# Kernel tuning notes

Measured on AMD Instinct MI355X. Metric: run time of the kernel, lower is better.

Reference implementation:

```python
import jax, jax.numpy as jnp
import numpy as np

DIM = 4096
HIDDEN = 11008
B, S = 4, 2048


def setup_inputs() -> dict:
    key = jax.random.key(0)
    k_x, k_g, k_u, k_d = jax.random.split(key, 4)
    x = jax.random.normal(k_x, (B, S, DIM), dtype=jnp.float32)
    # int8-range quantized weights, stored as int32 per spec (values in [-127, 127])
    w_gate = jax.random.randint(k_g, (HIDDEN, DIM), -127, 128, dtype=jnp.int32)
    w_up = jax.random.randint(k_u, (HIDDEN, DIM), -127, 128, dtype=jnp.int32)
    w_down = jax.random.randint(k_d, (DIM, HIDDEN), -127, 128, dtype=jnp.int32)
    # per-tensor scales (realistic small magnitudes)
    scale_gate = jnp.float32(0.01)
    scale_up = jnp.float32(0.01)
    scale_down = jnp.float32(0.01)
    return {
        "x": x,
        "w_gate": w_gate,
        "w_up": w_up,
        "w_down": w_down,
        "scale_gate": scale_gate,
        "scale_up": scale_up,
        "scale_down": scale_down,
    }


def _qlinear(x, w_int, scale):
    # faithful to QuantizedLinear.forward: dequantize then F.linear (x @ w.T)
    w = w_int.astype(x.dtype) * scale
    return jnp.einsum("bsd,hd->bsh", x, w)


def reference(x, w_gate, w_up, w_down, scale_gate, scale_up, scale_down):
    x_gate = _qlinear(x, w_gate, scale_gate)      # [B,S,HIDDEN]
    x_up = _qlinear(x, w_up, scale_up)            # [B,S,HIDDEN]
    x_mid = jax.nn.silu(x_gate) * x_up            # SwiGLU
    x_out = _qlinear(x_mid, w_down, scale_down)   # [B,S,DIM]
    return x_out
```

## Files before the change

### kernel.cpp

```cpp
#include <hip/hip_runtime.h>
#include <hip/hip_bf16.h>
#include <cstdint>
#include <cstddef>

#define DIM 4096
#define HIDDEN 11008
#define MTOK 8192

typedef __bf16 bf16x8 __attribute__((ext_vector_type(8)));
typedef float floatx4 __attribute__((ext_vector_type(4)));

__device__ __forceinline__ unsigned short f2bf(float f) {
    union { float f; unsigned int u; } v; v.f = f;
    unsigned int r = v.u + 0x7FFFu + ((v.u >> 16) & 1u);
    return (unsigned short)(r >> 16);
}

__device__ __forceinline__ void gload16(const void* g, void* l) {
    __builtin_amdgcn_global_load_lds(
        (const __attribute__((address_space(1))) unsigned int*)g,
        (__attribute__((address_space(3))) unsigned int*)l,
        16, 0, 0);
}

__device__ __forceinline__ floatx4 mfma16(bf16x8 a, bf16x8 b, floatx4 c) {
    return __builtin_amdgcn_mfma_f32_16x16x32_bf16(a, b, c, 0, 0, 0);
}


__global__ void cvt_f32_bf16(const float4* __restrict__ in, ushort4* __restrict__ out, int n4) {
    int i = blockIdx.x * 256 + threadIdx.x;
    if (i < n4) {
        float4 v = in[i];
        ushort4 o;
        o.x = f2bf(v.x); o.y = f2bf(v.y); o.z = f2bf(v.z); o.w = f2bf(v.w);
        out[i] = o;
    }
}

__global__ void cvt_i32_bf16(const int4* __restrict__ in, ushort4* __restrict__ out, int n4) {
    int i = blockIdx.x * 256 + threadIdx.x;
    if (i < n4) {
        int4 v = in[i];
        ushort4 o;
        o.x = f2bf((float)v.x); o.y = f2bf((float)v.y);
        o.z = f2bf((float)v.z); o.w = f2bf((float)v.w);
        out[i] = o;
    }
}

__global__ __launch_bounds__(256) void gemm_gateup(
    const unsigned short* __restrict__ A,
    const unsigned short* __restrict__ Bg,
    const unsigned short* __restrict__ Bu,
    unsigned short* __restrict__ mid,
    const float* __restrict__ sgp, const float* __restrict__ sup)
{
    __shared__ __align__(16) unsigned short sA[128 * 32];
    __shared__ __align__(16) unsigned short sBg[64 * 32];
    __shared__ __align__(16) unsigned short sBu[64 * 32];

    const int tid  = threadIdx.x;
    const int lane = tid & 63;
    const int wave = tid >> 6;
    const int wr   = wave >> 1;
    const int wc   = wave & 1;
    const int quad = lane >> 4;
    const int l16  = lane & 15;

    const size_t m0 = (size_t)blockIdx.x * 128;
    const size_t n0 = (size_t)blockIdx.y * 64;

    const int srow = tid >> 2;
    const int scol = (tid & 3) * 8;

    const unsigned short* gA0 = A  + (m0 + srow) * DIM + scol;
    const unsigned short* gA1 = gA0 + (size_t)64 * DIM;
    const unsigned short* gBg = Bg + (n0 + srow) * DIM + scol;
    const unsigned short* gBu = Bu + (n0 + srow) * DIM + scol;

    unsigned short* lA0 = &sA[tid * 8];
    unsigned short* lA1 = &sA[(tid + 256) * 8];
    unsigned short* lBg = &sBg[tid * 8];
    unsigned short* lBu = &sBu[tid * 8];

    const unsigned short* rA[4];
    const unsigned short* rBg[2];
    const unsigned short* rBu[2];
    for (int i = 0; i < 4; ++i)
        rA[i] = &sA[(wr * 64 + i * 16 + l16) * 32 + quad * 8];
    for (int j = 0; j < 2; ++j) {
        rBg[j] = &sBg[(wc * 32 + j * 16 + l16) * 32 + quad * 8];
        rBu[j] = &sBu[(wc * 32 + j * 16 + l16) * 32 + quad * 8];
    }

    floatx4 accg[4][2], accu[4][2];
    const floatx4 zero = {0.f, 0.f, 0.f, 0.f};
    for (int i = 0; i < 4; ++i)
        for (int j = 0; j < 2; ++j) { accg[i][j] = zero; accu[i][j] = zero; }

    for (int kt = 0; kt < DIM / 32; ++kt) {
        __syncthreads();
        gload16(gA0, lA0);
        gload16(gA1, lA1);
        gload16(gBg, lBg);
        gload16(gBu, lBu);
        gA0 += 32; gA1 += 32; gBg += 32; gBu += 32;
        __syncthreads();

        bf16x8 af[4], bg[2], bu[2];
        for (int i = 0; i < 4; ++i) af[i] = *(const bf16x8*)rA[i];
        for (int j = 0; j < 2; ++j) {
            bg[j] = *(const bf16x8*)rBg[j];
            bu[j] = *(const bf16x8*)rBu[j];
        }
        for (int i = 0; i < 4; ++i)
            for (int j = 0; j < 2; ++j) {
                accg[i][j] = mfma16(af[i], bg[j], accg[i][j]);
                accu[i][j] = mfma16(af[i], bu[j], accu[i][j]);
            }
    }

    const float s_g = *sgp;
    const float s_u = *sup;
    for (int i = 0; i < 4; ++i) {
        const size_t row = m0 + wr * 64 + i * 16 + quad * 4;
        for (int j = 0; j < 2; ++j) {
            const size_t col = n0 + wc * 32 + j * 16 + l16;
            for (int r = 0; r < 4; ++r) {
                float g = accg[i][j][r] * s_g;
                float u = accu[i][j][r] * s_u;
                float sig = 1.0f / (1.0f + __expf(-g));
                float v = g * sig * u;
                mid[(row + r) * HIDDEN + col] = f2bf(v);
            }
        }
    }
}

__global__ __launch_bounds__(256) void gemm_down(
    const unsigned short* __restrict__ A,
    const unsigned short* __restrict__ B,
    float* __restrict__ out,
    const float* __restrict__ sdp)
{
    __shared__ __align__(16) unsigned short sA[128 * 32];
    __shared__ __align__(16) unsigned short sB[128 * 32];

    const int tid  = threadIdx.x;
    const int lane = tid & 63;
    const int wave = tid >> 6;
    const int wr   = wave >> 1;
    const int wc   = wave & 1;
    const int quad = lane >> 4;
    const int l16  = lane & 15;

    const size_t m0 = (size_t)blockIdx.x * 128;
    const size_t n0 = (size_t)blockIdx.y * 128;

    const int srow = tid >> 2;
    const int scol = (tid & 3) * 8;

    const unsigned short* gA0 = A + (m0 + srow) * HIDDEN + scol;
    const unsigned short* gA1 = gA0 + (size_t)64 * HIDDEN;
    const unsigned short* gB0 = B + (n0 + srow) * HIDDEN + scol;
    const unsigned short* gB1 = gB0 + (size_t)64 * HIDDEN;

    unsigned short* lA0 = &sA[tid * 8];
    unsigned short* lA1 = &sA[(tid + 256) * 8];
    unsigned short* lB0 = &sB[tid * 8];
    unsigned short* lB1 = &sB[(tid + 256) * 8];

    const unsigned short* rA[4];
    const unsigned short* rB[4];
    for (int i = 0; i < 4; ++i) {
        rA[i] = &sA[(wr * 64 + i * 16 + l16) * 32 + quad * 8];
        rB[i] = &sB[(wc * 64 + i * 16 + l16) * 32 + quad * 8];
    }

    floatx4 acc[4][4];
    const floatx4 zero = {0.f, 0.f, 0.f, 0.f};
    for (int i = 0; i < 4; ++i)
        for (int j = 0; j < 4; ++j) acc[i][j] = zero;

    for (int kt = 0; kt < HIDDEN / 32; ++kt) {
        __syncthreads();
        gload16(gA0, lA0);
        gload16(gA1, lA1);
        gload16(gB0, lB0);
        gload16(gB1, lB1);
        gA0 += 32; gA1 += 32; gB0 += 32; gB1 += 32;
        __syncthreads();

        bf16x8 af[4], bf[4];
        for (int i = 0; i < 4; ++i) {
            af[i] = *(const bf16x8*)rA[i];
            bf[i] = *(const bf16x8*)rB[i];
        }
        for (int i = 0; i < 4; ++i)
            for (int j = 0; j < 4; ++j)
                acc[i][j] = mfma16(af[i], bf[j], acc[i][j]);
    }

    const float s_d = *sdp;
    for (int i = 0; i < 4; ++i) {
        const size_t row = m0 + wr * 64 + i * 16 + quad * 4;
        for (int j = 0; j < 4; ++j) {
            const size_t col = n0 + wc * 64 + j * 16 + l16;
            for (int r = 0; r < 4; ++r)
                out[(row + r) * DIM + col] = acc[i][j][r] * s_d;
        }
    }
}


extern "C" void kernel_launch(void* const* d_in, const int* in_sizes, int n_in,
                              void* d_out, int out_size, void* d_ws, size_t ws_size,
                              hipStream_t stream) {
    const float* x  = (const float*)d_in[0];
    const int*   wg = (const int*)d_in[1];
    const int*   wu = (const int*)d_in[2];
    const int*   wd = (const int*)d_in[3];
    const float* sg = (const float*)d_in[4];
    const float* su = (const float*)d_in[5];
    const float* sd = (const float*)d_in[6];
    float* out = (float*)d_out;

    unsigned short* xb   = (unsigned short*)d_ws;
    unsigned short* wgb  = xb  + (size_t)MTOK * DIM;
    unsigned short* wub  = wgb + (size_t)HIDDEN * DIM;
    unsigned short* wdb  = wub + (size_t)HIDDEN * DIM;
    unsigned short* midb = wdb + (size_t)DIM * HIDDEN;

    {
        int n4 = MTOK * DIM / 4;
        cvt_f32_bf16<<<dim3((n4 + 255) / 256), 256, 0, stream>>>((const float4*)x, (ushort4*)xb, n4);
    }
    {
        int n4 = HIDDEN * DIM / 4;
        cvt_i32_bf16<<<dim3((n4 + 255) / 256), 256, 0, stream>>>((const int4*)wg, (ushort4*)wgb, n4);
        cvt_i32_bf16<<<dim3((n4 + 255) / 256), 256, 0, stream>>>((const int4*)wu, (ushort4*)wub, n4);
        cvt_i32_bf16<<<dim3((n4 + 255) / 256), 256, 0, stream>>>((const int4*)wd, (ushort4*)wdb, n4);
    }

    gemm_gateup<<<dim3(MTOK / 128, HIDDEN / 64), 256, 0, stream>>>(xb, wgb, wub, midb, sg, su);

    gemm_down<<<dim3(MTOK / 128, DIM / 128), 256, 0, stream>>>(midb, wdb, out, sd);
}
```

Before: 3.269 ms.

## Use 256x256 tiles with 4-stage LDS pipeline and interleaved gate/up weights

Both GEMMs move to 512-thread blocks computing 256x256 tiles. They use a 4-deep circular LDS buffer filled by global_load_lds, with explicit vmcnt waits, barriers and s_setprio around the MFMA bursts, so loads overlap compute. Gate and up weights are interleaved in 16-row groups into one combined matrix, which lets the gate/up kernel run as a single GEMM and apply SwiGLU in its epilogue. The change also adds an XOR swizzle on LDS columns to avoid bank conflicts and a grouped block-index swizzle for L2 reuse. The cost is much higher LDS and register use per block, which lowers occupancy.

```diff
diff --git a/kernel.cpp b/kernel.cpp
--- a/kernel.cpp
+++ b/kernel.cpp
@@ -26,6 +26,13 @@
 __device__ __forceinline__ floatx4 mfma16(bf16x8 a, bf16x8 b, floatx4 c) {
     return __builtin_amdgcn_mfma_f32_16x16x32_bf16(a, b, c, 0, 0, 0);
 }
+
+#define FULL_BAR() do {                                   \
+    asm volatile("" ::: "memory");                        \
+    __builtin_amdgcn_s_barrier();                         \
+    asm volatile("" ::: "memory");                        \
+    __builtin_amdgcn_sched_barrier(0);                    \
+} while (0)
 
 
 __global__ void cvt_f32_bf16(const float4* __restrict__ in, ushort4* __restrict__ out, int n4) {
@@ -49,164 +56,232 @@
     }
 }
 
-__global__ __launch_bounds__(256) void gemm_gateup(
+__global__ void cvt_gateup(const int4* __restrict__ wg, const int4* __restrict__ wu,
+                           ushort4* __restrict__ outc, int n4) {
+    int i = blockIdx.x * 256 + threadIdx.x;
+    if (i < n4) {
+        const int rowc = i >> 10;
+        const int col4 = i & 1023;
+        const int srow = ((rowc >> 5) << 4) | (rowc & 15);
+        const int4* __restrict__ src = (rowc & 16) ? wu : wg;
+        int4 v = src[(size_t)srow * 1024 + col4];
+        ushort4 o;
+        o.x = f2bf((float)v.x); o.y = f2bf((float)v.y);
+        o.z = f2bf((float)v.z); o.w = f2bf((float)v.w);
+        outc[i] = o;
+    }
+}
+
+__global__ __launch_bounds__(512, 2) void gemm_gateup(
     const unsigned short* __restrict__ A,
-    const unsigned short* __restrict__ Bg,
-    const unsigned short* __restrict__ Bu,
+    const unsigned short* __restrict__ Bc,
     unsigned short* __restrict__ mid,
     const float* __restrict__ sgp, const float* __restrict__ sup)
 {
-    __shared__ __align__(16) unsigned short sA[128 * 32];
-    __shared__ __align__(16) unsigned short sBg[64 * 32];
-    __shared__ __align__(16) unsigned short sBu[64 * 32];
+    __shared__ __align__(16) unsigned short sA[4][256 * 32];
+    __shared__ __align__(16) unsigned short sB[4][256 * 32];
 
     const int tid  = threadIdx.x;
     const int lane = tid & 63;
     const int wave = tid >> 6;
-    const int wr   = wave >> 1;
-    const int wc   = wave & 1;
+    const int wr   = wave >> 2;
+    const int wc   = wave & 3;
     const int quad = lane >> 4;
     const int l16  = lane & 15;
 
-    const size_t m0 = (size_t)blockIdx.x * 128;
-    const size_t n0 = (size_t)blockIdx.y * 64;
-
-    const int srow = tid >> 2;
-    const int scol = (tid & 3) * 8;
-
-    const unsigned short* gA0 = A  + (m0 + srow) * DIM + scol;
-    const unsigned short* gA1 = gA0 + (size_t)64 * DIM;
-    const unsigned short* gBg = Bg + (n0 + srow) * DIM + scol;
-    const unsigned short* gBu = Bu + (n0 + srow) * DIM + scol;
-
-    unsigned short* lA0 = &sA[tid * 8];
-    unsigned short* lA1 = &sA[(tid + 256) * 8];
-    unsigned short* lBg = &sBg[tid * 8];
-    unsigned short* lBu = &sBu[tid * 8];
-
-    const unsigned short* rA[4];
-    const unsigned short* rBg[2];
-    const unsigned short* rBu[2];
-    for (int i = 0; i < 4; ++i)
-        rA[i] = &sA[(wr * 64 + i * 16 + l16) * 32 + quad * 8];
-    for (int j = 0; j < 2; ++j) {
-        rBg[j] = &sBg[(wc * 32 + j * 16 + l16) * 32 + quad * 8];
-        rBu[j] = &sBu[(wc * 32 + j * 16 + l16) * 32 + quad * 8];
-    }
-
-    floatx4 accg[4][2], accu[4][2];
+    const int cpx = (int)gridDim.x >> 3;
+    const int bid = blockIdx.x;
+    const int swz = (bid & 7) * cpx + (bid >> 3);
+    const int bm = swz & 31;
+    const int bn = swz >> 5;
+
+    const size_t m0 = (size_t)bm * 256;
+    const size_t n0 = (size_t)bn * 256;
+
+    const int r0 = tid >> 2;
+    const int c0 = (tid & 3) ^ ((r0 >> 1) & 3);
+    const unsigned short* gA0 = A  + (m0 + r0) * DIM + c0 * 8;
+    const unsigned short* gA1 = gA0 + (size_t)128 * DIM;
+    const unsigned short* gB0 = Bc + (n0 + r0) * DIM + c0 * 8;
+    const unsigned short* gB1 = gB0 + (size_t)128 * DIM;
+
+    const int co   = (quad ^ ((l16 >> 1) & 3)) * 8;
+    const int aoff = (wr * 128 + l16) * 32 + co;
+    const int boff = (wc * 64  + l16) * 32 + co;
+
+    floatx4 acc[8][4];
     const floatx4 zero = {0.f, 0.f, 0.f, 0.f};
-    for (int i = 0; i < 4; ++i)
-        for (int j = 0; j < 2; ++j) { accg[i][j] = zero; accu[i][j] = zero; }
-
-    for (int kt = 0; kt < DIM / 32; ++kt) {
-        __syncthreads();
-        gload16(gA0, lA0);
-        gload16(gA1, lA1);
-        gload16(gBg, lBg);
-        gload16(gBu, lBu);
-        gA0 += 32; gA1 += 32; gBg += 32; gBu += 32;
-        __syncthreads();
-
-        bf16x8 af[4], bg[2], bu[2];
-        for (int i = 0; i < 4; ++i) af[i] = *(const bf16x8*)rA[i];
-        for (int j = 0; j < 2; ++j) {
-            bg[j] = *(const bf16x8*)rBg[j];
-            bu[j] = *(const bf16x8*)rBu[j];
-        }
+#pragma unroll
+    for (int i = 0; i < 8; ++i)
+#pragma unroll
+        for (int j = 0; j < 4; ++j) acc[i][j] = zero;
+
+    auto STAGE = [&](int kt) {
+        const int s = kt & 3;
+        const size_t ko = (size_t)kt * 32;
+        gload16(gA0 + ko, &sA[s][tid * 8]);
+        gload16(gA1 + ko, &sA[s][(512 + tid) * 8]);
+        gload16(gB0 + ko, &sB[s][tid * 8]);
+        gload16(gB1 + ko, &sB[s][(512 + tid) * 8]);
+    };
+
+    STAGE(0); STAGE(1); STAGE(2);
+    asm volatile("s_waitcnt vmcnt(8)" ::: "memory");
+    FULL_BAR();
+
+    const int KT = DIM / 32;
+#pragma unroll 4
+    for (int kt = 0; kt < KT; ++kt) {
+        const unsigned short* pa = &sA[kt & 3][aoff];
+        const unsigned short* pb = &sB[kt & 3][boff];
+        bf16x8 a[4], b[4];
+#pragma unroll
+        for (int i = 0; i < 4; ++i) a[i] = *(const bf16x8*)(pa + i * 512);
+#pragma unroll
+        for (int j = 0; j < 4; ++j) b[j] = *(const bf16x8*)(pb + j * 512);
+        if (kt + 3 < KT) STAGE(kt + 3);
+        FULL_BAR();
+        __builtin_amdgcn_s_setprio(1);
+#pragma unroll
         for (int i = 0; i < 4; ++i)
-            for (int j = 0; j < 2; ++j) {
-                accg[i][j] = mfma16(af[i], bg[j], accg[i][j]);
-                accu[i][j] = mfma16(af[i], bu[j], accu[i][j]);
-            }
+#pragma unroll
+            for (int j = 0; j < 4; ++j)
+                acc[i][j] = mfma16(a[i], b[j], acc[i][j]);
+        __builtin_amdgcn_s_setprio(0);
+        FULL_BAR();
+#pragma unroll
+        for (int i = 0; i < 4; ++i) a[i] = *(const bf16x8*)(pa + 2048 + i * 512);
+        asm volatile("s_waitcnt vmcnt(8)" ::: "memory");
+        FULL_BAR();
+        __builtin_amdgcn_s_setprio(1);
+#pragma unroll
+        for (int i = 0; i < 4; ++i)
+#pragma unroll
+            for (int j = 0; j < 4; ++j)
+                acc[4 + i][j] = mfma16(a[i], b[j], acc[4 + i][j]);
+        __builtin_amdgcn_s_setprio(0);
+        FULL_BAR();
     }
 
     const float s_g = *sgp;
     const float s_u = *sup;
-    for (int i = 0; i < 4; ++i) {
-        const size_t row = m0 + wr * 64 + i * 16 + quad * 4;
-        for (int j = 0; j < 2; ++j) {
-            const size_t col = n0 + wc * 32 + j * 16 + l16;
+    const size_t colb = (n0 >> 1) + (size_t)wc * 32 + l16;
+#pragma unroll
+    for (int i = 0; i < 8; ++i) {
+        const size_t row = m0 + wr * 128 + i * 16 + quad * 4;
+#pragma unroll
+        for (int jj = 0; jj < 2; ++jj) {
+            const size_t col = colb + jj * 16;
+#pragma unroll
             for (int r = 0; r < 4; ++r) {
-                float g = accg[i][j][r] * s_g;
-                float u = accu[i][j][r] * s_u;
-                float sig = 1.0f / (1.0f + __expf(-g));
-                float v = g * sig * u;
+                float g = acc[i][2 * jj][r] * s_g;
+                float u = acc[i][2 * jj + 1][r] * s_u;
+                float v = g * u / (1.0f + __expf(-g));
                 mid[(row + r) * HIDDEN + col] = f2bf(v);
             }
         }
     }
 }
 
-__global__ __launch_bounds__(256) void gemm_down(
+__global__ __launch_bounds__(512, 2) void gemm_down(
     const unsigned short* __restrict__ A,
     const unsigned short* __restrict__ B,
     float* __restrict__ out,
     const float* __restrict__ sdp)
 {
-    __shared__ __align__(16) unsigned short sA[128 * 32];
-    __shared__ __align__(16) unsigned short sB[128 * 32];
+    __shared__ __align__(16) unsigned short sA[4][256 * 32];
+    __shared__ __align__(16) unsigned short sB[4][256 * 32];
 
     const int tid  = threadIdx.x;
     const int lane = tid & 63;
     const int wave = tid >> 6;
-    const int wr   = wave >> 1;
-    const int wc   = wave & 1;
+    const int wr   = wave >> 2;
+    const int wc   = wave & 3;
     const int quad = lane >> 4;
     const int l16  = lane & 15;
 
-    const size_t m0 = (size_t)blockIdx.x * 128;
-    const size_t n0 = (size_t)blockIdx.y * 128;
-
-    const int srow = tid >> 2;
-    const int scol = (tid & 3) * 8;
-
-    const unsigned short* gA0 = A + (m0 + srow) * HIDDEN + scol;
-    const unsigned short* gA1 = gA0 + (size_t)64 * HIDDEN;
-    const unsigned short* gB0 = B + (n0 + srow) * HIDDEN + scol;
-    const unsigned short* gB1 = gB0 + (size_t)64 * HIDDEN;
-
-    unsigned short* lA0 = &sA[tid * 8];
-    unsigned short* lA1 = &sA[(tid + 256) * 8];
-    unsigned short* lB0 = &sB[tid * 8];
-    unsigned short* lB1 = &sB[(tid + 256) * 8];
-
-    const unsigned short* rA[4];
-    const unsigned short* rB[4];
-    for (int i = 0; i < 4; ++i) {
-        rA[i] = &sA[(wr * 64 + i * 16 + l16) * 32 + quad * 8];
-        rB[i] = &sB[(wc * 64 + i * 16 + l16) * 32 + quad * 8];
-    }
-
-    floatx4 acc[4][4];
+    const int cpx = (int)gridDim.x >> 3;
+    const int bid = blockIdx.x;
+    const int swz = (bid & 7) * cpx + (bid >> 3);
+    const int bm = swz & 31;
+    const int bn = swz >> 5;
+
+    const size_t m0 = (size_t)bm * 256;
+    const size_t n0 = (size_t)bn * 256;
+
+    const int r0 = tid >> 2;
+    const int c0 = (tid & 3) ^ ((r0 >> 1) & 3);
+    const unsigned short* gA0 = A + (m0 + r0) * HIDDEN + c0 * 8;
+    const unsigned short* gA1 = gA0 + (size_t)128 * HIDDEN;
+    const unsigned short* gB0 = B + (n0 + r0) * HIDDEN + c0 * 8;
+    const unsigned short* gB1 = gB0 + (size_t)128 * HIDDEN;
+
+    const int co   = (quad ^ ((l16 >> 1) & 3)) * 8;
+    const int aoff = (wr * 128 + l16) * 32 + co;
+    const int boff = (wc * 64  + l16) * 32 + co;
+
+    floatx4 acc[8][4];
     const floatx4 zero = {0.f, 0.f, 0.f, 0.f};
-    for (int i = 0; i < 4; ++i)
+#pragma unroll
+    for (int i = 0; i < 8; ++i)
+#pragma unroll
         for (int j = 0; j < 4; ++j) acc[i][j] = zero;
 
-    for (int kt = 0; kt < HIDDEN / 32; ++kt) {
-        __syncthreads();
-        gload16(gA0, lA0);
-        gload16(gA1, lA1);
-        gload16(gB0, lB0);
-        gload16(gB1, lB1);
-        gA0 += 32; gA1 += 32; gB0 += 32; gB1 += 32;
-        __syncthreads();
-
-        bf16x8 af[4], bf[4];
-        for (int i = 0; i < 4; ++i) {
-            af[i] = *(const bf16x8*)rA[i];
-            bf[i] = *(const bf16x8*)rB[i];
-        }
+    auto STAGE = [&](int kt) {
+        const int s = kt & 3;
+        const size_t ko = (size_t)kt * 32;
+        gload16(gA0 + ko, &sA[s][tid * 8]);
+        gload16(gA1 + ko, &sA[s][(512 + tid) * 8]);
+        gload16(gB0 + ko, &sB[s][tid * 8]);
+        gload16(gB1 + ko, &sB[s][(512 + tid) * 8]);
+    };
+
+    STAGE(0); STAGE(1); STAGE(2);
+    asm volatile("s_waitcnt vmcnt(8)" ::: "memory");
+    FULL_BAR();
+
+    const int KT = HIDDEN / 32;
+#pragma unroll 4
+    for (int kt = 0; kt < KT; ++kt) {
+        const unsigned short* pa = &sA[kt & 3][aoff];
+        const unsigned short* pb = &sB[kt & 3][boff];
+        bf16x8 a[4], b[4];
+#pragma unroll
+        for (int i = 0; i < 4; ++i) a[i] = *(const bf16x8*)(pa + i * 512);
+#pragma unroll
+        for (int j = 0; j < 4; ++j) b[j] = *(const bf16x8*)(pb + j * 512);
+        if (kt + 3 < KT) STAGE(kt + 3);
+        FULL_BAR();
+        __builtin_amdgcn_s_setprio(1);
+#pragma unroll
         for (int i = 0; i < 4; ++i)
+#pragma unroll
             for (int j = 0; j < 4; ++j)
-                acc[i][j] = mfma16(af[i], bf[j], acc[i][j]);
+                acc[i][j] = mfma16(a[i], b[j], acc[i][j]);
+        __builtin_amdgcn_s_setprio(0);
+        FULL_BAR();
+#pragma unroll
+        for (int i = 0; i < 4; ++i) a[i] = *(const bf16x8*)(pa + 2048 + i * 512);
+        asm volatile("s_waitcnt vmcnt(8)" ::: "memory");
+        FULL_BAR();
+        __builtin_amdgcn_s_setprio(1);
+#pragma unroll
+        for (int i = 0; i < 4; ++i)
+#pragma unroll
+            for (int j = 0; j < 4; ++j)
+                acc[4 + i][j] = mfma16(a[i], b[j], acc[4 + i][j]);
+        __builtin_amdgcn_s_setprio(0);
+        FULL_BAR();
     }
 
     const float s_d = *sdp;
-    for (int i = 0; i < 4; ++i) {
-        const size_t row = m0 + wr * 64 + i * 16 + quad * 4;
+#pragma unroll
+    for (int i = 0; i < 8; ++i) {
+        const size_t row = m0 + wr * 128 + i * 16 + quad * 4;
+#pragma unroll
         for (int j = 0; j < 4; ++j) {
             const size_t col = n0 + wc * 64 + j * 16 + l16;
+#pragma unroll
             for (int r = 0; r < 4; ++r)
                 out[(row + r) * DIM + col] = acc[i][j][r] * s_d;
         }
@@ -227,9 +302,8 @@
     float* out = (float*)d_out;
 
     unsigned short* xb   = (unsigned short*)d_ws;
-    unsigned short* wgb  = xb  + (size_t)MTOK * DIM;
-    unsigned short* wub  = wgb + (size_t)HIDDEN * DIM;
-    unsigned short* wdb  = wub + (size_t)HIDDEN * DIM;
+    unsigned short* wcb  = xb  + (size_t)MTOK * DIM;
+    unsigned short* wdb  = wcb + (size_t)2 * HIDDEN * DIM;
     unsigned short* midb = wdb + (size_t)DIM * HIDDEN;
 
     {
@@ -237,13 +311,16 @@
         cvt_f32_bf16<<<dim3((n4 + 255) / 256), 256, 0, stream>>>((const float4*)x, (ushort4*)xb, n4);
     }
     {
-        int n4 = HIDDEN * DIM / 4;
-        cvt_i32_bf16<<<dim3((n4 + 255) / 256), 256, 0, stream>>>((const int4*)wg, (ushort4*)wgb, n4);
-        cvt_i32_bf16<<<dim3((n4 + 255) / 256), 256, 0, stream>>>((const int4*)wu, (ushort4*)wub, n4);
+        int n4 = 2 * HIDDEN * DIM / 4;
+        cvt_gateup<<<dim3((n4 + 255) / 256), 256, 0, stream>>>(
+            (const int4*)wg, (const int4*)wu, (ushort4*)wcb, n4);
+    }
+    {
+        int n4 = DIM * HIDDEN / 4;
         cvt_i32_bf16<<<dim3((n4 + 255) / 256), 256, 0, stream>>>((const int4*)wd, (ushort4*)wdb, n4);
     }
 
-    gemm_gateup<<<dim3(MTOK / 128, HIDDEN / 64), 256, 0, stream>>>(xb, wgb, wub, midb, sg, su);
-
-    gemm_down<<<dim3(MTOK / 128, DIM / 128), 256, 0, stream>>>(midb, wdb, out, sd);
-}
+    gemm_gateup<<<dim3((MTOK / 256) * (2 * HIDDEN / 256)), 512, 0, stream>>>(xb, wcb, midb, sg, su);
+
+    gemm_down<<<dim3((MTOK / 256) * (DIM / 256)), 512, 0, stream>>>(midb, wdb, out, sd);
+}
```

Result: no change. 3.226 ms (-1.3%).
